# Optimization experiments

Measured on AMD Instinct MI355X. Metric: run time of the kernel, lower is better.

The kernel has to match this reference:

```python
import jax, jax.numpy as jnp
import numpy as np

N_DIALOGS = 60
DIA_LEN = 100
N = N_DIALOGS * DIA_LEN  # 6000 utterances total
D_IN = 512
D_OUT = 512


def setup_inputs() -> dict:
    key = jax.random.key(0)
    k1, k2, k3, k4 = jax.random.split(key, 4)
    inputs = jax.random.normal(k1, (N, D_IN), dtype=jnp.float32)
    # per-dialog lengths (concrete host array; defines static graph structure)
    dia_len = np.full((N_DIALOGS,), DIA_LEN, dtype=np.int64)
    # one-hot speaker mask [N, 1, 2]; qmask[j,0,0]==1 -> speaker0 else speaker1
    sp = jax.random.randint(k2, (N,), 0, 2)
    qmask = jnp.zeros((N, 1, 2), jnp.int64).at[jnp.arange(N), 0, sp].set(1)
    W = jax.random.normal(k3, (D_OUT, D_IN), dtype=jnp.float32) / np.sqrt(D_IN)
    b = jax.random.normal(k4, (D_OUT,), dtype=jnp.float32) * 0.01
    return {"inputs": inputs, "dia_len": dia_len, "qmask": qmask, "W": W, "b": b}


def build_adj(inputs, dia_len, qmask):
    # Vectorized equivalent of message_passing_directed_speaker:
    # adj = I; edge (i,j) iff i,j in same dialog, same speaker, and consecutive
    # among that speaker's utterances; weight = 1 - arccos(clip(cos,-1,1))/pi.
    n = inputs.shape[0]
    dia_len_np = np.asarray(dia_len)
    did = jnp.asarray(np.repeat(np.arange(len(dia_len_np)), dia_len_np))  # dialog id per node
    sp0 = qmask[:, 0, 0] == 1  # True -> speaker0
    cs0 = jnp.cumsum(sp0.astype(jnp.int32))
    cs1 = jnp.cumsum((~sp0).astype(jnp.int32))
    csel = jnp.where(sp0, cs0, cs1)  # running count of own speaker
    idx = jnp.arange(n)
    # j>i, same dialog, same speaker, no same-speaker utterance strictly between
    upper = ((did[None, :] == did[:, None])
             & (sp0[None, :] == sp0[:, None])
             & (csel[None, :] - csel[:, None] == 1)
             & (idx[None, :] > idx[:, None]))
    edge = upper | upper.T
    # pairwise cosine similarity (cossim returns 0 when a norm is 0)
    nrm = jnp.sqrt(jnp.sum(inputs * inputs, axis=-1))  # [N]
    denom = nrm[:, None] * nrm[None, :]
    dots = inputs @ inputs.T  # [N, N]
    cos = jnp.where(denom > 0, dots / jnp.where(denom > 0, denom, 1.0), 0.0)
    cos_safe = jnp.where(edge, jnp.clip(cos, -1.0, 1.0), 0.0)
    w = 1.0 - jnp.arccos(cos_safe) / jnp.pi
    return jnp.where(edge, w, 0.0) + jnp.eye(n, dtype=inputs.dtype)


def reference(inputs, dia_len, qmask, W, b):
    adj = build_adj(inputs, dia_len, qmask)  # [N, N]
    x = adj @ inputs                          # [N, D_IN]
    return x @ W.T + b                        # [N, D_OUT]
```

## Files before the change

### kernel.cpp

```cpp
#include <hip/hip_runtime.h>
#include <hip/hip_bf16.h>

#define N_NODES 6000
#define DIA     100
#define DDIM    512
#define LDA     520

typedef short short8   __attribute__((ext_vector_type(8)));
typedef float floatx4  __attribute__((ext_vector_type(4)));

__device__ __forceinline__ unsigned short f2bf(float f) {
    unsigned int u = __float_as_uint(f);
    unsigned int r = (u + 0x7fffu + ((u >> 16) & 1u)) >> 16;
    return (unsigned short)r;
}

__device__ __forceinline__ float wave_reduce_sum(float v) {
    #pragma unroll
    for (int off = 32; off > 0; off >>= 1) v += __shfl_xor(v, off, 64);
    return v;
}

__global__ __launch_bounds__(512) void wcast_kernel(
    const float* __restrict__ W, unsigned short* __restrict__ wbf)
{
    int base = blockIdx.x * 4096 + threadIdx.x * 8;
    float4 a = *(const float4*)(W + base);
    float4 b = *(const float4*)(W + base + 4);
    union { unsigned short u[8]; short8 v; } o;
    o.u[0]=f2bf(a.x); o.u[1]=f2bf(a.y); o.u[2]=f2bf(a.z); o.u[3]=f2bf(a.w);
    o.u[4]=f2bf(b.x); o.u[5]=f2bf(b.y); o.u[6]=f2bf(b.z); o.u[7]=f2bf(b.w);
    *(short8*)(wbf + base) = o.v;
}

__global__ __launch_bounds__(512) void fused_kernel(
    const float* __restrict__ x, const int* __restrict__ qmask,
    const unsigned short* __restrict__ wbf, const float* __restrict__ bias,
    float* __restrict__ out)
{
    __shared__ unsigned short As[64 * LDA];
    __shared__ int sp_s[200];
    __shared__ int nxt_s[64];
    __shared__ int prv_s[64];

    int tid = threadIdx.x;
    int wv = tid >> 6, lane = tid & 63;
    int m0 = blockIdx.x * 64;

    int dia_lo = (m0 / DIA) * DIA;
    int dia_hi = ((m0 + 63) / DIA) * DIA + DIA;
    if (dia_hi > N_NODES) dia_hi = N_NODES;
    int range = dia_hi - dia_lo;
    if (tid < range) sp_s[tid] = qmask[2 * (dia_lo + tid)];
    __syncthreads();

    if (tid < 64) {
        int i = m0 + tid;
        int nx = -1, pv = -1;
        if (i < N_NODES) {
            int li = i - dia_lo;
            int ds = (i / DIA) * DIA - dia_lo;
            int de = ds + DIA;
            int sp = sp_s[li];
            for (int q = li + 1; q < de; ++q) if (sp_s[q] == sp) { nx = q + dia_lo; break; }
            for (int q = li - 1; q >= ds; --q) if (sp_s[q] == sp) { pv = q + dia_lo; break; }
        }
        nxt_s[tid] = nx; prv_s[tid] = pv;
    }
    __syncthreads();

    for (int t = 0; t < 8; ++t) {
        int rr = wv * 8 + t;
        int i = m0 + rr;
        unsigned short* dst = As + rr * LDA + lane * 8;
        if (i >= N_NODES) {
            *(short8*)dst = (short8)0;
            continue;
        }
        int j = nxt_s[rr];
        int p = prv_s[rr];
        const float* ri = x + (size_t)i * DDIM + lane * 8;
        float4 xa = *(const float4*)(ri);
        float4 xb = *(const float4*)(ri + 4);
        float ni = xa.x*xa.x + xa.y*xa.y + xa.z*xa.z + xa.w*xa.w
                 + xb.x*xb.x + xb.y*xb.y + xb.z*xb.z + xb.w*xb.w;
        float dj = 0.0f, nj = 0.0f, dp = 0.0f, np = 0.0f;
        float4 ja, jb, pa, pb;
        if (j >= 0) {
            const float* rj = x + (size_t)j * DDIM + lane * 8;
            ja = *(const float4*)(rj);
            jb = *(const float4*)(rj + 4);
            dj = xa.x*ja.x + xa.y*ja.y + xa.z*ja.z + xa.w*ja.w
               + xb.x*jb.x + xb.y*jb.y + xb.z*jb.z + xb.w*jb.w;
            nj = ja.x*ja.x + ja.y*ja.y + ja.z*ja.z + ja.w*ja.w
               + jb.x*jb.x + jb.y*jb.y + jb.z*jb.z + jb.w*jb.w;
        }
        if (p >= 0) {
            const float* rp = x + (size_t)p * DDIM + lane * 8;
            pa = *(const float4*)(rp);
            pb = *(const float4*)(rp + 4);
            dp = xa.x*pa.x + xa.y*pa.y + xa.z*pa.z + xa.w*pa.w
               + xb.x*pb.x + xb.y*pb.y + xb.z*pb.z + xb.w*pb.w;
            np = pa.x*pa.x + pa.y*pa.y + pa.z*pa.z + pa.w*pa.w
               + pb.x*pb.x + pb.y*pb.y + pb.z*pb.z + pb.w*pb.w;
        }
        ni = wave_reduce_sum(ni);
        dj = wave_reduce_sum(dj);
        nj = wave_reduce_sum(nj);
        dp = wave_reduce_sum(dp);
        np = wave_reduce_sum(np);

        float wx = 0.0f, wp = 0.0f;
        if (j >= 0) {
            float dn = ni * nj;
            float c = (dn > 0.0f) ? (dj * __frsqrt_rn(dn)) : 0.0f;
            c = fminf(1.0f, fmaxf(-1.0f, c));
            wx = 1.0f - acosf(c) * 0.3183098861837907f;
        }
        if (p >= 0) {
            float dn = np * ni;
            float c = (dn > 0.0f) ? (dp * __frsqrt_rn(dn)) : 0.0f;
            c = fminf(1.0f, fmaxf(-1.0f, c));
            wp = 1.0f - acosf(c) * 0.3183098861837907f;
        }

        float acc[8];
        acc[0]=xa.x; acc[1]=xa.y; acc[2]=xa.z; acc[3]=xa.w;
        acc[4]=xb.x; acc[5]=xb.y; acc[6]=xb.z; acc[7]=xb.w;
        if (j >= 0) {
            acc[0]+=wx*ja.x; acc[1]+=wx*ja.y; acc[2]+=wx*ja.z; acc[3]+=wx*ja.w;
            acc[4]+=wx*jb.x; acc[5]+=wx*jb.y; acc[6]+=wx*jb.z; acc[7]+=wx*jb.w;
        }
        if (p >= 0) {
            acc[0]+=wp*pa.x; acc[1]+=wp*pa.y; acc[2]+=wp*pa.z; acc[3]+=wp*pa.w;
            acc[4]+=wp*pb.x; acc[5]+=wp*pb.y; acc[6]+=wp*pb.z; acc[7]+=wp*pb.w;
        }
        union { unsigned short u[8]; short8 v; } o;
        #pragma unroll
        for (int q = 0; q < 8; ++q) o.u[q] = f2bf(acc[q]);
        *(short8*)dst = o.v;
    }
    __syncthreads();

    int n0 = blockIdx.y * 256 + wv * 32;
    int fr = lane & 15;
    int kq = (lane >> 4) * 8;
    floatx4 acc[4][2] = {};
    const unsigned short* As_base = As + fr * LDA + kq;
    const unsigned short* bb = wbf + (size_t)(n0 + fr) * DDIM + kq;

    #pragma unroll 2
    for (int k = 0; k < DDIM; k += 32) {
        short8 af[4], bfv[2];
        #pragma unroll
        for (int ms = 0; ms < 4; ++ms)
            af[ms] = *(const short8*)(As_base + ms * 16 * LDA + k);
        #pragma unroll
        for (int ns = 0; ns < 2; ++ns)
            bfv[ns] = *(const short8*)(bb + (size_t)ns * 16 * DDIM + k);
        #pragma unroll
        for (int ms = 0; ms < 4; ++ms)
            #pragma unroll
            for (int ns = 0; ns < 2; ++ns)
                acc[ms][ns] = __builtin_amdgcn_mfma_f32_16x16x32_bf16(
                    af[ms], bfv[ns], acc[ms][ns], 0, 0, 0);
    }

    int col = lane & 15;
    int rbase = (lane >> 4) * 4;
    #pragma unroll
    for (int ms = 0; ms < 4; ++ms) {
        #pragma unroll
        for (int ns = 0; ns < 2; ++ns) {
            int n = n0 + ns * 16 + col;
            float bv = bias[n];
            #pragma unroll
            for (int r = 0; r < 4; ++r) {
                int m = m0 + ms * 16 + rbase + r;
                if (m < N_NODES)
                    out[(size_t)m * DDIM + n] = acc[ms][ns][r] + bv;
            }
        }
    }
}

extern "C" void kernel_launch(void* const* d_in, const int* in_sizes, int n_in,
                              void* d_out, int out_size, void* d_ws, size_t ws_size,
                              hipStream_t stream) {
    const float* inputs = (const float*)d_in[0];
    const int* qmask   = (const int*)d_in[2];
    const float* W     = (const float*)d_in[3];
    const float* bias  = (const float*)d_in[4];
    float* out = (float*)d_out;

    unsigned short* wbf = (unsigned short*)d_ws;

    wcast_kernel<<<dim3(64),    512, 0, stream>>>(W, wbf);
    fused_kernel<<<dim3(94, 2), 512, 0, stream>>>(inputs, qmask, wbf, bias, out);
}
```

Measured before the change: 95.83 us.

## Split fused aggregation+GEMM into parallel prep kernel and small-tile GEMM

Moves the neighbor aggregation out of the GEMM into a prep kernel that runs one wave per node and writes bf16 rows to workspace. Neighbor search now uses wave ballots instead of a serial scan, and the W cast is folded into the same launch. The GEMM reads its A operand from global memory with 32x32 tiles per wave across 752 blocks, for far more parallelism than the previous 188 blocks. The cost is an extra global round trip of the aggregated bf16 matrix and no LDS staging, so operands are re-read from L2.

```diff
diff --git a/kernel.cpp b/kernel.cpp
--- a/kernel.cpp
+++ b/kernel.cpp
@@ -4,7 +4,7 @@
 #define N_NODES 6000
 #define DIA     100
 #define DDIM    512
-#define LDA     520
+#define NPAD    6016
 
 typedef short short8   __attribute__((ext_vector_type(8)));
 typedef float floatx4  __attribute__((ext_vector_type(4)));
@@ -21,155 +21,151 @@
     return v;
 }
 
-__global__ __launch_bounds__(512) void wcast_kernel(
-    const float* __restrict__ W, unsigned short* __restrict__ wbf)
+__global__ __launch_bounds__(256) void prep_kernel(
+    const float* __restrict__ x, const int* __restrict__ qmask,
+    const float* __restrict__ W, unsigned short* __restrict__ xbf,
+    unsigned short* __restrict__ wbf)
 {
-    int base = blockIdx.x * 4096 + threadIdx.x * 8;
-    float4 a = *(const float4*)(W + base);
-    float4 b = *(const float4*)(W + base + 4);
+    int bid = blockIdx.x;
+    int tid = threadIdx.x;
+    if (bid >= N_NODES / 4) {
+        int cb = bid - N_NODES / 4;
+        if (cb < 128) {
+            int base = cb * 2048 + tid * 8;
+            float4 a = *(const float4*)(W + base);
+            float4 b = *(const float4*)(W + base + 4);
+            union { unsigned short u[8]; short8 v; } o;
+            o.u[0]=f2bf(a.x); o.u[1]=f2bf(a.y); o.u[2]=f2bf(a.z); o.u[3]=f2bf(a.w);
+            o.u[4]=f2bf(b.x); o.u[5]=f2bf(b.y); o.u[6]=f2bf(b.z); o.u[7]=f2bf(b.w);
+            *(short8*)(wbf + base) = o.v;
+        } else {
+            short8 z = (short8)0;
+            #pragma unroll
+            for (int t = 0; t < 4; ++t)
+                *(short8*)(xbf + (size_t)N_NODES * DDIM + (t * 256 + tid) * 8) = z;
+        }
+        return;
+    }
+    int wv = tid >> 6, lane = tid & 63;
+    int i = bid * 4 + wv;
+    int sp = qmask[2 * i];
+    int dstart = (i / DIA) * DIA;
+    int dend   = dstart + DIA;
+
+    int cand = i + 1 + lane;
+    unsigned long long b1 = __ballot(cand < dend && qmask[2 * cand] == sp);
+    int j = -1;
+    if (b1) j = i + __ffsll(b1);
+    else {
+        int c2 = i + 65 + lane;
+        unsigned long long b2 = __ballot(lane < 35 && c2 < dend && qmask[2 * c2] == sp);
+        if (b2) j = i + 64 + __ffsll(b2);
+    }
+    int candp = i - 1 - lane;
+    unsigned long long p1 = __ballot(candp >= dstart && qmask[2 * candp] == sp);
+    int p = -1;
+    if (p1) p = i - __ffsll(p1);
+    else {
+        int pc2 = i - 65 - lane;
+        unsigned long long p2 = __ballot(lane < 35 && pc2 >= dstart && qmask[2 * pc2] == sp);
+        if (p2) p = i - 64 - __ffsll(p2);
+    }
+
+    const float* ri = x + (size_t)i * DDIM + lane * 8;
+    float4 xa = *(const float4*)(ri);
+    float4 xb = *(const float4*)(ri + 4);
+    float ni = xa.x*xa.x + xa.y*xa.y + xa.z*xa.z + xa.w*xa.w
+             + xb.x*xb.x + xb.y*xb.y + xb.z*xb.z + xb.w*xb.w;
+    float dj = 0.0f, nj = 0.0f, dp = 0.0f, np = 0.0f;
+    float4 ja, jb, pa, pb;
+    if (j >= 0) {
+        const float* rj = x + (size_t)j * DDIM + lane * 8;
+        ja = *(const float4*)(rj);
+        jb = *(const float4*)(rj + 4);
+        dj = xa.x*ja.x + xa.y*ja.y + xa.z*ja.z + xa.w*ja.w
+           + xb.x*jb.x + xb.y*jb.y + xb.z*jb.z + xb.w*jb.w;
+        nj = ja.x*ja.x + ja.y*ja.y + ja.z*ja.z + ja.w*ja.w
+           + jb.x*jb.x + jb.y*jb.y + jb.z*jb.z + jb.w*jb.w;
+    }
+    if (p >= 0) {
+        const float* rp = x + (size_t)p * DDIM + lane * 8;
+        pa = *(const float4*)(rp);
+        pb = *(const float4*)(rp + 4);
+        dp = xa.x*pa.x + xa.y*pa.y + xa.z*pa.z + xa.w*pa.w
+           + xb.x*pb.x + xb.y*pb.y + xb.z*pb.z + xb.w*pb.w;
+        np = pa.x*pa.x + pa.y*pa.y + pa.z*pa.z + pa.w*pa.w
+           + pb.x*pb.x + pb.y*pb.y + pb.z*pb.z + pb.w*pb.w;
+    }
+    ni = wave_reduce_sum(ni);
+    dj = wave_reduce_sum(dj);
+    nj = wave_reduce_sum(nj);
+    dp = wave_reduce_sum(dp);
+    np = wave_reduce_sum(np);
+
+    float wx = 0.0f, wp = 0.0f;
+    if (j >= 0) {
+        float dn = ni * nj;
+        float c = (dn > 0.0f) ? (dj * __frsqrt_rn(dn)) : 0.0f;
+        c = fminf(1.0f, fmaxf(-1.0f, c));
+        wx = 1.0f - acosf(c) * 0.3183098861837907f;
+    }
+    if (p >= 0) {
+        float dn = np * ni;
+        float c = (dn > 0.0f) ? (dp * __frsqrt_rn(dn)) : 0.0f;
+        c = fminf(1.0f, fmaxf(-1.0f, c));
+        wp = 1.0f - acosf(c) * 0.3183098861837907f;
+    }
+
+    float acc[8];
+    acc[0]=xa.x; acc[1]=xa.y; acc[2]=xa.z; acc[3]=xa.w;
+    acc[4]=xb.x; acc[5]=xb.y; acc[6]=xb.z; acc[7]=xb.w;
+    if (j >= 0) {
+        acc[0]+=wx*ja.x; acc[1]+=wx*ja.y; acc[2]+=wx*ja.z; acc[3]+=wx*ja.w;
+        acc[4]+=wx*jb.x; acc[5]+=wx*jb.y; acc[6]+=wx*jb.z; acc[7]+=wx*jb.w;
+    }
+    if (p >= 0) {
+        acc[0]+=wp*pa.x; acc[1]+=wp*pa.y; acc[2]+=wp*pa.z; acc[3]+=wp*pa.w;
+        acc[4]+=wp*pb.x; acc[5]+=wp*pb.y; acc[6]+=wp*pb.z; acc[7]+=wp*pb.w;
+    }
     union { unsigned short u[8]; short8 v; } o;
-    o.u[0]=f2bf(a.x); o.u[1]=f2bf(a.y); o.u[2]=f2bf(a.z); o.u[3]=f2bf(a.w);
-    o.u[4]=f2bf(b.x); o.u[5]=f2bf(b.y); o.u[6]=f2bf(b.z); o.u[7]=f2bf(b.w);
-    *(short8*)(wbf + base) = o.v;
+    #pragma unroll
+    for (int q = 0; q < 8; ++q) o.u[q] = f2bf(acc[q]);
+    *(short8*)(xbf + (size_t)i * DDIM + lane * 8) = o.v;
 }
 
-__global__ __launch_bounds__(512) void fused_kernel(
-    const float* __restrict__ x, const int* __restrict__ qmask,
-    const unsigned short* __restrict__ wbf, const float* __restrict__ bias,
-    float* __restrict__ out)
+__global__ __launch_bounds__(256) void gemm_kernel(
+    const unsigned short* __restrict__ xbf, const unsigned short* __restrict__ wbf,
+    const float* __restrict__ bias, float* __restrict__ out)
 {
-    __shared__ unsigned short As[64 * LDA];
-    __shared__ int sp_s[200];
-    __shared__ int nxt_s[64];
-    __shared__ int prv_s[64];
-
-    int tid = threadIdx.x;
-    int wv = tid >> 6, lane = tid & 63;
-    int m0 = blockIdx.x * 64;
-
-    int dia_lo = (m0 / DIA) * DIA;
-    int dia_hi = ((m0 + 63) / DIA) * DIA + DIA;
-    if (dia_hi > N_NODES) dia_hi = N_NODES;
-    int range = dia_hi - dia_lo;
-    if (tid < range) sp_s[tid] = qmask[2 * (dia_lo + tid)];
-    __syncthreads();
-
-    if (tid < 64) {
-        int i = m0 + tid;
-        int nx = -1, pv = -1;
-        if (i < N_NODES) {
-            int li = i - dia_lo;
-            int ds = (i / DIA) * DIA - dia_lo;
-            int de = ds + DIA;
-            int sp = sp_s[li];
-            for (int q = li + 1; q < de; ++q) if (sp_s[q] == sp) { nx = q + dia_lo; break; }
-            for (int q = li - 1; q >= ds; --q) if (sp_s[q] == sp) { pv = q + dia_lo; break; }
-        }
-        nxt_s[tid] = nx; prv_s[tid] = pv;
-    }
-    __syncthreads();
-
-    for (int t = 0; t < 8; ++t) {
-        int rr = wv * 8 + t;
-        int i = m0 + rr;
-        unsigned short* dst = As + rr * LDA + lane * 8;
-        if (i >= N_NODES) {
-            *(short8*)dst = (short8)0;
-            continue;
-        }
-        int j = nxt_s[rr];
-        int p = prv_s[rr];
-        const float* ri = x + (size_t)i * DDIM + lane * 8;
-        float4 xa = *(const float4*)(ri);
-        float4 xb = *(const float4*)(ri + 4);
-        float ni = xa.x*xa.x + xa.y*xa.y + xa.z*xa.z + xa.w*xa.w
-                 + xb.x*xb.x + xb.y*xb.y + xb.z*xb.z + xb.w*xb.w;
-        float dj = 0.0f, nj = 0.0f, dp = 0.0f, np = 0.0f;
-        float4 ja, jb, pa, pb;
-        if (j >= 0) {
-            const float* rj = x + (size_t)j * DDIM + lane * 8;
-            ja = *(const float4*)(rj);
-            jb = *(const float4*)(rj + 4);
-            dj = xa.x*ja.x + xa.y*ja.y + xa.z*ja.z + xa.w*ja.w
-               + xb.x*jb.x + xb.y*jb.y + xb.z*jb.z + xb.w*jb.w;
-            nj = ja.x*ja.x + ja.y*ja.y + ja.z*ja.z + ja.w*ja.w
-               + jb.x*jb.x + jb.y*jb.y + jb.z*jb.z + jb.w*jb.w;
-        }
-        if (p >= 0) {
-            const float* rp = x + (size_t)p * DDIM + lane * 8;
-            pa = *(const float4*)(rp);
-            pb = *(const float4*)(rp + 4);
-            dp = xa.x*pa.x + xa.y*pa.y + xa.z*pa.z + xa.w*pa.w
-               + xb.x*pb.x + xb.y*pb.y + xb.z*pb.z + xb.w*pb.w;
-            np = pa.x*pa.x + pa.y*pa.y + pa.z*pa.z + pa.w*pa.w
-               + pb.x*pb.x + pb.y*pb.y + pb.z*pb.z + pb.w*pb.w;
-        }
-        ni = wave_reduce_sum(ni);
-        dj = wave_reduce_sum(dj);
-        nj = wave_reduce_sum(nj);
-        dp = wave_reduce_sum(dp);
-        np = wave_reduce_sum(np);
-
-        float wx = 0.0f, wp = 0.0f;
-        if (j >= 0) {
-            float dn = ni * nj;
-            float c = (dn > 0.0f) ? (dj * __frsqrt_rn(dn)) : 0.0f;
-            c = fminf(1.0f, fmaxf(-1.0f, c));
-            wx = 1.0f - acosf(c) * 0.3183098861837907f;
-        }
-        if (p >= 0) {
-            float dn = np * ni;
-            float c = (dn > 0.0f) ? (dp * __frsqrt_rn(dn)) : 0.0f;
-            c = fminf(1.0f, fmaxf(-1.0f, c));
-            wp = 1.0f - acosf(c) * 0.3183098861837907f;
-        }
-
-        float acc[8];
-        acc[0]=xa.x; acc[1]=xa.y; acc[2]=xa.z; acc[3]=xa.w;
-        acc[4]=xb.x; acc[5]=xb.y; acc[6]=xb.z; acc[7]=xb.w;
-        if (j >= 0) {
-            acc[0]+=wx*ja.x; acc[1]+=wx*ja.y; acc[2]+=wx*ja.z; acc[3]+=wx*ja.w;
-            acc[4]+=wx*jb.x; acc[5]+=wx*jb.y; acc[6]+=wx*jb.z; acc[7]+=wx*jb.w;
-        }
-        if (p >= 0) {
-            acc[0]+=wp*pa.x; acc[1]+=wp*pa.y; acc[2]+=wp*pa.z; acc[3]+=wp*pa.w;
-            acc[4]+=wp*pb.x; acc[5]+=wp*pb.y; acc[6]+=wp*pb.z; acc[7]+=wp*pb.w;
-        }
-        union { unsigned short u[8]; short8 v; } o;
-        #pragma unroll
-        for (int q = 0; q < 8; ++q) o.u[q] = f2bf(acc[q]);
-        *(short8*)dst = o.v;
-    }
-    __syncthreads();
-
-    int n0 = blockIdx.y * 256 + wv * 32;
+    int g = blockIdx.x * 4 + (threadIdx.x >> 6);
+    int lane = threadIdx.x & 63;
+    int m0 = (g >> 4) * 32;
+    int n0 = (g & 15) * 32;
     int fr = lane & 15;
     int kq = (lane >> 4) * 8;
-    floatx4 acc[4][2] = {};
-    const unsigned short* As_base = As + fr * LDA + kq;
-    const unsigned short* bb = wbf + (size_t)(n0 + fr) * DDIM + kq;
 
-    #pragma unroll 2
+    const unsigned short* a0p = xbf + (size_t)(m0 + fr) * DDIM + kq;
+    const unsigned short* a1p = a0p + 16 * DDIM;
+    const unsigned short* b0p = wbf + (size_t)(n0 + fr) * DDIM + kq;
+    const unsigned short* b1p = b0p + 16 * DDIM;
+
+    floatx4 acc[2][2] = {};
+    #pragma unroll 4
     for (int k = 0; k < DDIM; k += 32) {
-        short8 af[4], bfv[2];
-        #pragma unroll
-        for (int ms = 0; ms < 4; ++ms)
-            af[ms] = *(const short8*)(As_base + ms * 16 * LDA + k);
-        #pragma unroll
-        for (int ns = 0; ns < 2; ++ns)
-            bfv[ns] = *(const short8*)(bb + (size_t)ns * 16 * DDIM + k);
-        #pragma unroll
-        for (int ms = 0; ms < 4; ++ms)
-            #pragma unroll
-            for (int ns = 0; ns < 2; ++ns)
-                acc[ms][ns] = __builtin_amdgcn_mfma_f32_16x16x32_bf16(
-                    af[ms], bfv[ns], acc[ms][ns], 0, 0, 0);
+        short8 a0 = *(const short8*)(a0p + k);
+        short8 a1 = *(const short8*)(a1p + k);
+        short8 b0 = *(const short8*)(b0p + k);
+        short8 b1 = *(const short8*)(b1p + k);
+        acc[0][0] = __builtin_amdgcn_mfma_f32_16x16x32_bf16(a0, b0, acc[0][0], 0, 0, 0);
+        acc[0][1] = __builtin_amdgcn_mfma_f32_16x16x32_bf16(a0, b1, acc[0][1], 0, 0, 0);
+        acc[1][0] = __builtin_amdgcn_mfma_f32_16x16x32_bf16(a1, b0, acc[1][0], 0, 0, 0);
+        acc[1][1] = __builtin_amdgcn_mfma_f32_16x16x32_bf16(a1, b1, acc[1][1], 0, 0, 0);
     }
 
     int col = lane & 15;
     int rbase = (lane >> 4) * 4;
     #pragma unroll
-    for (int ms = 0; ms < 4; ++ms) {
+    for (int ms = 0; ms < 2; ++ms) {
         #pragma unroll
         for (int ns = 0; ns < 2; ++ns) {
             int n = n0 + ns * 16 + col;
@@ -193,8 +189,10 @@
     const float* bias  = (const float*)d_in[4];
     float* out = (float*)d_out;
 
-    unsigned short* wbf = (unsigned short*)d_ws;
+    char* ws = (char*)d_ws;
+    unsigned short* xbf = (unsigned short*)ws;
+    unsigned short* wbf = xbf + (size_t)NPAD * DDIM;
 
-    wcast_kernel<<<dim3(64),    512, 0, stream>>>(W, wbf);
-    fused_kernel<<<dim3(94, 2), 512, 0, stream>>>(inputs, qmask, wbf, bias, out);
+    prep_kernel<<<dim3(N_NODES / 4 + 129), 256, 0, stream>>>(inputs, qmask, W, xbf, wbf);
+    gemm_kernel<<<dim3(752),               256, 0, stream>>>(xbf, wbf, bias, out);
 }
```

Result: slower. 99.61 us (+3.9%).

## Halve row tile, fuse W bf16 cast into GEMM, restructure cosine reductions

Applied to the files above, without the earlier changes.

Drops the separate W-cast kernel and converts fp32 W to bf16 inside the MFMA loop. The M tile shrinks from 64 to 32 rows, so the grid doubles to 188x2 blocks. The row-similarity stage now uses 16 threads per row with shared-memory partial sums instead of wave shuffles. This removes one launch and raises block count, at the cost of reading fp32 W (twice the bytes) and redoing the conversion in every block, plus lower MFMA reuse per block.

```diff
diff --git a/kernel.cpp b/kernel.cpp
--- a/kernel.cpp
+++ b/kernel.cpp
@@ -4,6 +4,7 @@
 #define N_NODES 6000
 #define DIA     100
 #define DDIM    512
+#define NT      32
 #define LDA     520
 
 typedef short short8   __attribute__((ext_vector_type(8)));
@@ -11,56 +12,43 @@
 
 __device__ __forceinline__ unsigned short f2bf(float f) {
     unsigned int u = __float_as_uint(f);
-    unsigned int r = (u + 0x7fffu + ((u >> 16) & 1u)) >> 16;
-    return (unsigned short)r;
-}
-
-__device__ __forceinline__ float wave_reduce_sum(float v) {
-    #pragma unroll
-    for (int off = 32; off > 0; off >>= 1) v += __shfl_xor(v, off, 64);
-    return v;
-}
-
-__global__ __launch_bounds__(512) void wcast_kernel(
-    const float* __restrict__ W, unsigned short* __restrict__ wbf)
-{
-    int base = blockIdx.x * 4096 + threadIdx.x * 8;
-    float4 a = *(const float4*)(W + base);
-    float4 b = *(const float4*)(W + base + 4);
+    return (unsigned short)((u + 0x7fffu + ((u >> 16) & 1u)) >> 16);
+}
+
+__device__ __forceinline__ short8 pack_bf8(float4 a, float4 b) {
     union { unsigned short u[8]; short8 v; } o;
     o.u[0]=f2bf(a.x); o.u[1]=f2bf(a.y); o.u[2]=f2bf(a.z); o.u[3]=f2bf(a.w);
     o.u[4]=f2bf(b.x); o.u[5]=f2bf(b.y); o.u[6]=f2bf(b.z); o.u[7]=f2bf(b.w);
-    *(short8*)(wbf + base) = o.v;
+    return o.v;
 }
 
 __global__ __launch_bounds__(512) void fused_kernel(
     const float* __restrict__ x, const int* __restrict__ qmask,
-    const unsigned short* __restrict__ wbf, const float* __restrict__ bias,
+    const float* __restrict__ W, const float* __restrict__ bias,
     float* __restrict__ out)
 {
-    __shared__ unsigned short As[64 * LDA];
-    __shared__ int sp_s[200];
-    __shared__ int nxt_s[64];
-    __shared__ int prv_s[64];
+    __shared__ __align__(16) char smem_raw[NT * LDA * 2];
+    unsigned short* As = (unsigned short*)smem_raw;
+    float* part = (float*)smem_raw;
+    __shared__ float red[5 * NT];
+    __shared__ float wnx_s[NT], wnp_s[NT];
+    __shared__ int   sp_s[224];
+    __shared__ int   nxt_s[NT], prv_s[NT];
 
     int tid = threadIdx.x;
-    int wv = tid >> 6, lane = tid & 63;
-    int m0 = blockIdx.x * 64;
+    int m0 = blockIdx.x * NT;
 
     int dia_lo = (m0 / DIA) * DIA;
-    int dia_hi = ((m0 + 63) / DIA) * DIA + DIA;
-    if (dia_hi > N_NODES) dia_hi = N_NODES;
+    int lastr = m0 + NT - 1; if (lastr >= N_NODES) lastr = N_NODES - 1;
+    int dia_hi = (lastr / DIA) * DIA + DIA;
     int range = dia_hi - dia_lo;
     if (tid < range) sp_s[tid] = qmask[2 * (dia_lo + tid)];
     __syncthreads();
-
-    if (tid < 64) {
-        int i = m0 + tid;
-        int nx = -1, pv = -1;
+    if (tid < NT) {
+        int i = m0 + tid; int nx = -1, pv = -1;
         if (i < N_NODES) {
             int li = i - dia_lo;
-            int ds = (i / DIA) * DIA - dia_lo;
-            int de = ds + DIA;
+            int ds = (i / DIA) * DIA - dia_lo, de = ds + DIA;
             int sp = sp_s[li];
             for (int q = li + 1; q < de; ++q) if (sp_s[q] == sp) { nx = q + dia_lo; break; }
             for (int q = li - 1; q >= ds; --q) if (sp_s[q] == sp) { pv = q + dia_lo; break; }
@@ -69,116 +57,133 @@
     }
     __syncthreads();
 
-    for (int t = 0; t < 8; ++t) {
-        int rr = wv * 8 + t;
-        int i = m0 + rr;
-        unsigned short* dst = As + rr * LDA + lane * 8;
-        if (i >= N_NODES) {
-            *(short8*)dst = (short8)0;
-            continue;
-        }
-        int j = nxt_s[rr];
-        int p = prv_s[rr];
-        const float* ri = x + (size_t)i * DDIM + lane * 8;
-        float4 xa = *(const float4*)(ri);
-        float4 xb = *(const float4*)(ri + 4);
-        float ni = xa.x*xa.x + xa.y*xa.y + xa.z*xa.z + xa.w*xa.w
-                 + xb.x*xb.x + xb.y*xb.y + xb.z*xb.z + xb.w*xb.w;
-        float dj = 0.0f, nj = 0.0f, dp = 0.0f, np = 0.0f;
-        float4 ja, jb, pa, pb;
-        if (j >= 0) {
-            const float* rj = x + (size_t)j * DDIM + lane * 8;
-            ja = *(const float4*)(rj);
-            jb = *(const float4*)(rj + 4);
-            dj = xa.x*ja.x + xa.y*ja.y + xa.z*ja.z + xa.w*ja.w
-               + xb.x*jb.x + xb.y*jb.y + xb.z*jb.z + xb.w*jb.w;
-            nj = ja.x*ja.x + ja.y*ja.y + ja.z*ja.z + ja.w*ja.w
-               + jb.x*jb.x + jb.y*jb.y + jb.z*jb.z + jb.w*jb.w;
-        }
-        if (p >= 0) {
-            const float* rp = x + (size_t)p * DDIM + lane * 8;
-            pa = *(const float4*)(rp);
-            pb = *(const float4*)(rp + 4);
-            dp = xa.x*pa.x + xa.y*pa.y + xa.z*pa.z + xa.w*pa.w
-               + xb.x*pb.x + xb.y*pb.y + xb.z*pb.z + xb.w*pb.w;
-            np = pa.x*pa.x + pa.y*pa.y + pa.z*pa.z + pa.w*pa.w
-               + pb.x*pb.x + pb.y*pb.y + pb.z*pb.z + pb.w*pb.w;
-        }
-        ni = wave_reduce_sum(ni);
-        dj = wave_reduce_sum(dj);
-        nj = wave_reduce_sum(nj);
-        dp = wave_reduce_sum(dp);
-        np = wave_reduce_sum(np);
-
-        float wx = 0.0f, wp = 0.0f;
-        if (j >= 0) {
-            float dn = ni * nj;
-            float c = (dn > 0.0f) ? (dj * __frsqrt_rn(dn)) : 0.0f;
-            c = fminf(1.0f, fmaxf(-1.0f, c));
-            wx = 1.0f - acosf(c) * 0.3183098861837907f;
-        }
-        if (p >= 0) {
-            float dn = np * ni;
-            float c = (dn > 0.0f) ? (dp * __frsqrt_rn(dn)) : 0.0f;
-            c = fminf(1.0f, fmaxf(-1.0f, c));
-            wp = 1.0f - acosf(c) * 0.3183098861837907f;
-        }
-
-        float acc[8];
-        acc[0]=xa.x; acc[1]=xa.y; acc[2]=xa.z; acc[3]=xa.w;
-        acc[4]=xb.x; acc[5]=xb.y; acc[6]=xb.z; acc[7]=xb.w;
-        if (j >= 0) {
-            acc[0]+=wx*ja.x; acc[1]+=wx*ja.y; acc[2]+=wx*ja.z; acc[3]+=wx*ja.w;
-            acc[4]+=wx*jb.x; acc[5]+=wx*jb.y; acc[6]+=wx*jb.z; acc[7]+=wx*jb.w;
-        }
-        if (p >= 0) {
-            acc[0]+=wp*pa.x; acc[1]+=wp*pa.y; acc[2]+=wp*pa.z; acc[3]+=wp*pa.w;
-            acc[4]+=wp*pb.x; acc[5]+=wp*pb.y; acc[6]+=wp*pb.z; acc[7]+=wp*pb.w;
-        }
-        union { unsigned short u[8]; short8 v; } o;
+    int r = tid >> 4, c = tid & 15;
+    int i = m0 + r;
+    int j = nxt_s[r], p = prv_s[r];
+    const float* bi = x + (size_t)(i < N_NODES ? i : 0) * DDIM + c * 8;
+    const float* bj = x + (size_t)(j >= 0 ? j : 0) * DDIM + c * 8;
+    const float* bp = x + (size_t)(p >= 0 ? p : 0) * DDIM + c * 8;
+    float ni = 0.f, dj = 0.f, nj = 0.f, dp = 0.f, np = 0.f;
+    #pragma unroll
+    for (int t = 0; t < 4; ++t) {
+        float4 a0 = *(const float4*)(bi + t * 128);
+        float4 a1 = *(const float4*)(bi + t * 128 + 4);
+        float4 j0 = *(const float4*)(bj + t * 128);
+        float4 j1 = *(const float4*)(bj + t * 128 + 4);
+        float4 p0 = *(const float4*)(bp + t * 128);
+        float4 p1 = *(const float4*)(bp + t * 128 + 4);
+        ni += a0.x*a0.x + a0.y*a0.y + a0.z*a0.z + a0.w*a0.w
+            + a1.x*a1.x + a1.y*a1.y + a1.z*a1.z + a1.w*a1.w;
+        dj += a0.x*j0.x + a0.y*j0.y + a0.z*j0.z + a0.w*j0.w
+            + a1.x*j1.x + a1.y*j1.y + a1.z*j1.z + a1.w*j1.w;
+        nj += j0.x*j0.x + j0.y*j0.y + j0.z*j0.z + j0.w*j0.w
+            + j1.x*j1.x + j1.y*j1.y + j1.z*j1.z + j1.w*j1.w;
+        dp += a0.x*p0.x + a0.y*p0.y + a0.z*p0.z + a0.w*p0.w
+            + a1.x*p1.x + a1.y*p1.y + a1.z*p1.z + a1.w*p1.w;
+        np += p0.x*p0.x + p0.y*p0.y + p0.z*p0.z + p0.w*p0.w
+            + p1.x*p1.x + p1.y*p1.y + p1.z*p1.z + p1.w*p1.w;
+    }
+    int pidx = r * 17 + c;
+    part[0 * 544 + pidx] = ni;
+    part[1 * 544 + pidx] = dj;
+    part[2 * 544 + pidx] = nj;
+    part[3 * 544 + pidx] = dp;
+    part[4 * 544 + pidx] = np;
+    __syncthreads();
+
+    if (tid < 160) {
+        int a = tid >> 5, rr = tid & 31;
+        const float* pp = part + a * 544 + rr * 17;
+        float s = 0.f;
         #pragma unroll
-        for (int q = 0; q < 8; ++q) o.u[q] = f2bf(acc[q]);
-        *(short8*)dst = o.v;
-    }
-    __syncthreads();
-
+        for (int q = 0; q < 16; ++q) s += pp[q];
+        red[a * NT + rr] = s;
+    }
+    __syncthreads();
+    if (tid < NT) {
+        float rni = red[tid],          rdj = red[NT + tid], rnj = red[2 * NT + tid],
+              rdp = red[3 * NT + tid], rnp = red[4 * NT + tid];
+        float wx = 0.f, wp = 0.f;
+        if (nxt_s[tid] >= 0) {
+            float dn = rni * rnj;
+            float cc = (dn > 0.f) ? (rdj * __frsqrt_rn(dn)) : 0.f;
+            cc = fminf(1.f, fmaxf(-1.f, cc));
+            wx = 1.f - acosf(cc) * 0.3183098861837907f;
+        }
+        if (prv_s[tid] >= 0) {
+            float dn = rnp * rni;
+            float cc = (dn > 0.f) ? (rdp * __frsqrt_rn(dn)) : 0.f;
+            cc = fminf(1.f, fmaxf(-1.f, cc));
+            wp = 1.f - acosf(cc) * 0.3183098861837907f;
+        }
+        wnx_s[tid] = wx; wnp_s[tid] = wp;
+    }
+    __syncthreads();
+
+    {
+        float wx = wnx_s[r], wp = wnp_s[r];
+        unsigned short* dst = As + r * LDA + c * 8;
+        bool valid = (i < N_NODES);
+        #pragma unroll
+        for (int t = 0; t < 4; ++t) {
+            short8 v8;
+            if (valid) {
+                float4 a0 = *(const float4*)(bi + t * 128);
+                float4 a1 = *(const float4*)(bi + t * 128 + 4);
+                float4 j0 = *(const float4*)(bj + t * 128);
+                float4 j1 = *(const float4*)(bj + t * 128 + 4);
+                float4 p0 = *(const float4*)(bp + t * 128);
+                float4 p1 = *(const float4*)(bp + t * 128 + 4);
+                a0.x += wx * j0.x + wp * p0.x;  a0.y += wx * j0.y + wp * p0.y;
+                a0.z += wx * j0.z + wp * p0.z;  a0.w += wx * j0.w + wp * p0.w;
+                a1.x += wx * j1.x + wp * p1.x;  a1.y += wx * j1.y + wp * p1.y;
+                a1.z += wx * j1.z + wp * p1.z;  a1.w += wx * j1.w + wp * p1.w;
+                v8 = pack_bf8(a0, a1);
+            } else {
+                v8 = (short8)0;
+            }
+            *(short8*)(dst + t * 128) = v8;
+        }
+    }
+    __syncthreads();
+
+    int wv = tid >> 6, lane = tid & 63;
     int n0 = blockIdx.y * 256 + wv * 32;
     int fr = lane & 15;
     int kq = (lane >> 4) * 8;
-    floatx4 acc[4][2] = {};
-    const unsigned short* As_base = As + fr * LDA + kq;
-    const unsigned short* bb = wbf + (size_t)(n0 + fr) * DDIM + kq;
-
+    const unsigned short* As_b = As + fr * LDA + kq;
+    const float* w0p = W + (size_t)(n0 + fr) * DDIM + kq;
+    const float* w1p = w0p + 16 * DDIM;
+    floatx4 acc[2][2] = {};
     #pragma unroll 2
     for (int k = 0; k < DDIM; k += 32) {
-        short8 af[4], bfv[2];
-        #pragma unroll
-        for (int ms = 0; ms < 4; ++ms)
-            af[ms] = *(const short8*)(As_base + ms * 16 * LDA + k);
-        #pragma unroll
-        for (int ns = 0; ns < 2; ++ns)
-            bfv[ns] = *(const short8*)(bb + (size_t)ns * 16 * DDIM + k);
-        #pragma unroll
-        for (int ms = 0; ms < 4; ++ms)
-            #pragma unroll
-            for (int ns = 0; ns < 2; ++ns)
-                acc[ms][ns] = __builtin_amdgcn_mfma_f32_16x16x32_bf16(
-                    af[ms], bfv[ns], acc[ms][ns], 0, 0, 0);
+        short8 a0 = *(const short8*)(As_b + k);
+        short8 a1 = *(const short8*)(As_b + 16 * LDA + k);
+        float4 wa0 = *(const float4*)(w0p + k);
+        float4 wb0 = *(const float4*)(w0p + k + 4);
+        float4 wa1 = *(const float4*)(w1p + k);
+        float4 wb1 = *(const float4*)(w1p + k + 4);
+        short8 b0 = pack_bf8(wa0, wb0);
+        short8 b1 = pack_bf8(wa1, wb1);
+        acc[0][0] = __builtin_amdgcn_mfma_f32_16x16x32_bf16(a0, b0, acc[0][0], 0, 0, 0);
+        acc[0][1] = __builtin_amdgcn_mfma_f32_16x16x32_bf16(a0, b1, acc[0][1], 0, 0, 0);
+        acc[1][0] = __builtin_amdgcn_mfma_f32_16x16x32_bf16(a1, b0, acc[1][0], 0, 0, 0);
+        acc[1][1] = __builtin_amdgcn_mfma_f32_16x16x32_bf16(a1, b1, acc[1][1], 0, 0, 0);
     }
 
     int col = lane & 15;
     int rbase = (lane >> 4) * 4;
     #pragma unroll
-    for (int ms = 0; ms < 4; ++ms) {
+    for (int ms = 0; ms < 2; ++ms) {
         #pragma unroll
         for (int ns = 0; ns < 2; ++ns) {
             int n = n0 + ns * 16 + col;
             float bv = bias[n];
             #pragma unroll
-            for (int r = 0; r < 4; ++r) {
-                int m = m0 + ms * 16 + rbase + r;
+            for (int rr = 0; rr < 4; ++rr) {
+                int m = m0 + ms * 16 + rbase + rr;
                 if (m < N_NODES)
-                    out[(size_t)m * DDIM + n] = acc[ms][ns][r] + bv;
+                    out[(size_t)m * DDIM + n] = acc[ms][ns][rr] + bv;
             }
         }
     }
@@ -193,8 +198,5 @@
     const float* bias  = (const float*)d_in[4];
     float* out = (float*)d_out;
 
-    unsigned short* wbf = (unsigned short*)d_ws;
-
-    wcast_kernel<<<dim3(64),    512, 0, stream>>>(W, wbf);
-    fused_kernel<<<dim3(94, 2), 512, 0, stream>>>(inputs, qmask, wbf, bias, out);
-}
+    fused_kernel<<<dim3(188, 2), 512, 0, stream>>>(inputs, qmask, W, bias, out);
+}
```

New measurement: 107.9 us. +12.6%, slower.
